# Kernel optimization log

Measured on AMD Instinct MI355X. Metric: run time of the kernel, lower is better.

## Reference

```python
import jax, jax.numpy as jnp
import numpy as np

N = 100000   # nodes
E = 1600000  # edges
IN = 128     # in_node_channels
H = 128      # hidden_channels
EPS = 1e-5   # BatchNorm eps


def _gcn_conv(x, W, b, src, dst, n):
    # x' = W x, then symmetric-normalized aggregation with self-loops (PyG GCNConv)
    xw = x @ W                                             # [N, H]
    loop = jnp.arange(n, dtype=src.dtype)
    src_f = jnp.concatenate([src, loop])                   # [E+N]
    dst_f = jnp.concatenate([dst, loop])
    deg = jax.ops.segment_sum(jnp.ones(src_f.shape, xw.dtype), dst_f, num_segments=n)
    dis = jax.lax.rsqrt(jnp.maximum(deg, 1.0))             # deg >= 1 due to self-loops
    norm = dis[src_f] * dis[dst_f]                         # [E+N]
    msg = xw[src_f] * norm[:, None]                        # gather + scale
    out = jax.ops.segment_sum(msg, dst_f, num_segments=n)  # scatter-add
    return out + b


def _bn(x, gamma, beta):
    # training-mode BatchNorm1d over the node dimension
    m = jnp.mean(x, axis=0)
    v = jnp.mean(jnp.square(x - m), axis=0)
    return gamma * (x - m) * jax.lax.rsqrt(v + EPS) + beta


def setup_inputs() -> dict:
    key = jax.random.key(0)
    ks = jax.random.split(key, 8)
    glorot = lambda k, shape, fan: jax.random.normal(k, shape, jnp.float32) / np.sqrt(fan).astype(np.float32)
    x = jax.random.normal(ks[0], (N, IN), jnp.float32)
    edge_index = jax.random.randint(ks[1], (2, E), 0, N, dtype=jnp.int32)
    return {
        "x": x,
        "edge_index": edge_index,
        "W1": glorot(ks[2], (IN, H), IN), "b1": jnp.zeros((H,), jnp.float32),
        "g1": jnp.ones((H,), jnp.float32), "be1": jnp.zeros((H,), jnp.float32),
        "W2": glorot(ks[3], (H, H), H), "b2": jnp.zeros((H,), jnp.float32),
        "g2": jnp.ones((H,), jnp.float32), "be2": jnp.zeros((H,), jnp.float32),
        "Wm1": glorot(ks[4], (H, 64), H), "bm1": jnp.zeros((64,), jnp.float32),
        "Wm2": glorot(ks[5], (64, 1), 64), "bm2": jnp.zeros((1,), jnp.float32),
    }


def reference(x, edge_index, W1, b1, g1, be1, W2, b2, g2, be2, Wm1, bm1, Wm2, bm2):
    src, dst = edge_index[0], edge_index[1]
    h = jax.nn.relu(_bn(_gcn_conv(x, W1, b1, src, dst, N), g1, be1))
    h = jax.nn.relu(_bn(_gcn_conv(h, W2, b2, src, dst, N), g2, be2))
    # MLP head (dropout is identity in eval / deterministic reference)
    h = jax.nn.relu(h @ Wm1 + bm1)
    out = h @ Wm2 + bm2                                     # [N, 1]
    return jnp.squeeze(out, axis=-1)                        # [N]
```

## Files before the change

kernel.cpp:

```cpp
#include <hip/hip_runtime.h>
#include <hip/hip_fp16.h>

#define HC 128
#define EPS_BN 1e-5f
#define NSTRIPE 8
#define AGG_BLOCKS 3072
#define BSHIFT 9
#define BNODES (1 << BSHIFT)
#define BCAP 12288
#define CHUNK 8192
#define SRC_BITS 18

typedef _Float16 f16;
typedef f16  f16x8 __attribute__((ext_vector_type(8)));
typedef float f32x4 __attribute__((ext_vector_type(4)));

__global__ __launch_bounds__(1024) void init_small(int* __restrict__ gcur,
                                                   float* __restrict__ stats,
                                                   f16* __restrict__ padrow) {
    int tid = threadIdx.x;
    if (tid < 256) gcur[tid] = tid * BCAP;
    if (tid < 128) padrow[tid] = (f16)0.f;
    for (int i = tid; i < 2 * NSTRIPE * 256; i += 1024) stats[i] = 0.f;
}

__global__ __launch_bounds__(1024) void edge_bin(const int* __restrict__ src,
                                                 const int* __restrict__ dst,
                                                 int* __restrict__ gcur,
                                                 unsigned int* __restrict__ packed, int E) {
    __shared__ int cnt[256];
    __shared__ int cur[256];
    const int tid = threadIdx.x;
    const int e0 = blockIdx.x * CHUNK;
    int dreg[8];
    if (tid < 256) cnt[tid] = 0;
    __syncthreads();
#pragma unroll
    for (int i = 0; i < 8; ++i) {
        int e = e0 + i * 1024 + tid;
        dreg[i] = (e < E) ? dst[e] : -1;
        if (dreg[i] >= 0) atomicAdd(&cnt[dreg[i] >> BSHIFT], 1);
    }
    __syncthreads();
    if (tid < 256) cur[tid] = (cnt[tid] > 0) ? atomicAdd(&gcur[tid], cnt[tid]) : 0;
    __syncthreads();
#pragma unroll
    for (int i = 0; i < 8; ++i) {
        int e = e0 + i * 1024 + tid;
        if (dreg[i] >= 0) {
            int s = src[e];
            int pos = atomicAdd(&cur[dreg[i] >> BSHIFT], 1);
            packed[pos] = ((unsigned)(dreg[i] & (BNODES - 1)) << SRC_BITS) | (unsigned)s;
        }
    }
}

__global__ __launch_bounds__(1024) void sort_wprep(const unsigned int* __restrict__ packed,
                                                   const int* __restrict__ gcur,
                                                   int2* __restrict__ rowptr2,
                                                   float* __restrict__ dis,
                                                   int* __restrict__ srcs, int n, int nbSort,
                                                   const float* __restrict__ W1,
                                                   const float* __restrict__ W2,
                                                   const float* __restrict__ Wm1,
                                                   f16* __restrict__ Wt1,
                                                   f16* __restrict__ Wt2,
                                                   f16* __restrict__ Wm1t) {
    if (blockIdx.x >= nbSort) {
        int idx = (blockIdx.x - nbSort) * 1024 + threadIdx.x;
        if (idx < 16384) {
            int k = idx >> 7, c = idx & 127;
            Wt1[(size_t)c * HC + k] = (f16)W1[idx];
        } else if (idx < 32768) {
            int i = idx - 16384;
            int k = i >> 7, c = i & 127;
            Wt2[(size_t)c * HC + k] = (f16)W2[i];
        } else if (idx < 40960) {
            int i = idx - 32768;
            int c = i >> 7, k = i & 127;
            Wm1t[(size_t)c * HC + k] = (f16)Wm1[(size_t)k * 64 + c];
        }
        return;
    }
    __shared__ int cnt[BNODES];
    __shared__ int cur[BNODES];
    __shared__ int scn[BNODES];
    const int b = blockIdx.x;
    const int node0 = b << BSHIFT;
    const int tid = threadIdx.x;
    const int base = b * BCAP;
    const int end  = gcur[b];

    if (tid < BNODES) cnt[tid] = 0;
    __syncthreads();
    for (int e = base + tid; e < end; e += 1024)
        atomicAdd(&cnt[packed[e] >> SRC_BITS], 1);
    __syncthreads();
    if (tid < BNODES) scn[tid] = cnt[tid];
    __syncthreads();
    for (int off = 1; off < BNODES; off <<= 1) {
        int t = 0;
        if (tid < BNODES && tid >= off) t = scn[tid - off];
        __syncthreads();
        if (tid < BNODES) scn[tid] += t;
        __syncthreads();
    }
    if (tid < BNODES) {
        int excl = scn[tid] - cnt[tid];
        int node = node0 + tid;
        if (node < n) {
            rowptr2[node] = make_int2(base + excl, base + excl + cnt[tid]);
            dis[node] = rsqrtf((float)cnt[tid] + 1.f);
        }
        cur[tid] = excl;
    }
    __syncthreads();
    for (int e = base + tid; e < end; e += 1024) {
        unsigned p = packed[e];
        int pos = atomicAdd(&cur[p >> SRC_BITS], 1);
        srcs[base + pos] = (int)(p & ((1u << SRC_BITS) - 1));
    }
}

template<int SRC_F16, int TRANS>
__global__ __launch_bounds__(512) void gemm_mfma(const void* __restrict__ Xv,
                                                 const f16* __restrict__ Wt,
                                                 const float* __restrict__ stats,
                                                 const float* __restrict__ gamma,
                                                 const float* __restrict__ beta,
                                                 const float* __restrict__ dis,
                                                 f16* __restrict__ Y, int n) {
    __shared__ f16 Ah[128][136];
    __shared__ f16 Bh[128][136];
    __shared__ float sc[HC], sh[HC];
    const int tid  = threadIdx.x;
    const int row0 = blockIdx.x * 128;

    if constexpr (TRANS) {
        if (tid < 128) {
            float s = 0.f, q = 0.f;
#pragma unroll
            for (int t = 0; t < NSTRIPE; ++t) {
                s += stats[t * 256 + tid];
                q += stats[t * 256 + 128 + tid];
            }
            float m = s / (float)n;
            float v = q / (float)n - m * m;
            float scv = gamma[tid] * rsqrtf(fmaxf(v, 0.f) + EPS_BN);
            sc[tid] = scv;
            sh[tid] = beta[tid] - m * scv;
        }
    }

#pragma unroll
    for (int i = 0; i < 4; ++i) {
        int idx = i * 512 + tid;
        int r = idx >> 4, g = idx & 15;
        *(f16x8*)&Bh[r][g * 8] = *(const f16x8*)(Wt + (size_t)r * HC + g * 8);
    }
    __syncthreads();

#pragma unroll
    for (int i = 0; i < 4; ++i) {
        int idx = i * 512 + tid;
        int r = idx >> 4, g = idx & 15;
        int grow = row0 + r;
        f16x8 h = {};
        if (grow < n) {
            if constexpr (SRC_F16) {
                f16x8 v = *(const f16x8*)((const f16*)Xv + (size_t)grow * HC + g * 8);
                if constexpr (TRANS) {
#pragma unroll
                    for (int j = 0; j < 8; ++j) {
                        float f = (float)v[j];
                        f = fmaxf(fmaf(f, sc[g * 8 + j], sh[g * 8 + j]), 0.f);
                        h[j] = (f16)f;
                    }
                } else h = v;
            } else {
                const float* X = (const float*)Xv;
                float4 a = *(const float4*)(X + (size_t)grow * HC + g * 8);
                float4 c = *(const float4*)(X + (size_t)grow * HC + g * 8 + 4);
                h[0] = (f16)a.x; h[1] = (f16)a.y; h[2] = (f16)a.z; h[3] = (f16)a.w;
                h[4] = (f16)c.x; h[5] = (f16)c.y; h[6] = (f16)c.z; h[7] = (f16)c.w;
            }
        }
        *(f16x8*)&Ah[r][g * 8] = h;
    }
    __syncthreads();

    const int wv   = tid >> 6;
    const int lane = tid & 63;
    const int m    = lane & 15;
    const int kq   = (lane >> 4) * 8;

    f32x4 acc[8] = {};
#pragma unroll
    for (int kc = 0; kc < HC; kc += 32) {
        f16x8 a = *(const f16x8*)&Ah[wv * 16 + m][kc + kq];
#pragma unroll
        for (int t = 0; t < 8; ++t) {
            f16x8 b = *(const f16x8*)&Bh[t * 16 + m][kc + kq];
            acc[t] = __builtin_amdgcn_mfma_f32_16x16x32_f16(a, b, acc[t], 0, 0, 0);
        }
    }

    __syncthreads();
    {
        const int rg = (lane >> 4) * 4;
        float dv[4];
#pragma unroll
        for (int r = 0; r < 4; ++r) {
            int grow = row0 + wv * 16 + rg + r;
            dv[r] = (grow < n) ? dis[grow] : 0.f;
        }
#pragma unroll
        for (int t = 0; t < 8; ++t)
#pragma unroll
            for (int r = 0; r < 4; ++r)
                Ah[wv * 16 + rg + r][t * 16 + m] = (f16)(acc[t][r] * dv[r]);
    }
    __syncthreads();
#pragma unroll
    for (int i = 0; i < 4; ++i) {
        int idx = i * 512 + tid;
        int r = idx >> 4, g = idx & 15;
        int grow = row0 + r;
        if (grow < n)
            *(f16x8*)(Y + (size_t)grow * HC + g * 8) = *(const f16x8*)&Ah[r][g * 8];
    }
}

__global__ __launch_bounds__(256) void gcn_agg_f16(const f16* __restrict__ xws,
                                                   const int* __restrict__ srcs,
                                                   const int2* __restrict__ rowptr2,
                                                   const float* __restrict__ dis,
                                                   const float* __restrict__ bias,
                                                   f16* __restrict__ out,
                                                   float* __restrict__ stats,
                                                   int n, int nwaves) {
    __shared__ float lds_s[4][128], lds_q[4][128];
    const int wv   = threadIdx.x >> 6;
    const int lane = threadIdx.x & 63;
    const int g    = lane >> 4;
    const int cg   = lane & 15;

    float b8[8];
#pragma unroll
    for (int j = 0; j < 8; ++j) b8[j] = bias[cg * 8 + j];

    float s8[8] = {}, q8[8] = {};

    for (int node = blockIdx.x * 4 + wv; node < n; node += nwaves) {
        const int2 rp = rowptr2[node];
        const int e1 = rp.y;
        float acc[8] = {};
        int e  = rp.x;
        int i0 = e + g, i1 = i0 + 4;
        int s0 = (i0 < e1) ? srcs[i0] : n;
        int s1 = (i1 < e1) ? srcs[i1] : n;
        while (e < e1) {
            int en = e + 8;
            int j0 = en + g, j1 = j0 + 4;
            int t0 = (j0 < e1) ? srcs[j0] : n;
            int t1 = (j1 < e1) ? srcs[j1] : n;
            f16x8 v0 = *(const f16x8*)(xws + (size_t)s0 * HC + cg * 8);
            f16x8 v1 = *(const f16x8*)(xws + (size_t)s1 * HC + cg * 8);
#pragma unroll
            for (int j = 0; j < 8; ++j) {
                acc[j] += (float)v0[j];
                acc[j] += (float)v1[j];
            }
            s0 = t0; s1 = t1; e = en;
        }
#pragma unroll
        for (int j = 0; j < 8; ++j) acc[j] += __shfl_xor(acc[j], 16);
#pragma unroll
        for (int j = 0; j < 8; ++j) acc[j] += __shfl_xor(acc[j], 32);

        if (g == 0) {
            float dv = dis[node];
            f16x8 self = *(const f16x8*)(xws + (size_t)node * HC + cg * 8);
            f16x8 o;
#pragma unroll
            for (int j = 0; j < 8; ++j) {
                float r = fmaf(acc[j] + (float)self[j], dv, b8[j]);
                o[j] = (f16)r;
                s8[j] += r;
                q8[j] += r * r;
            }
            *(f16x8*)(out + (size_t)node * HC + cg * 8) = o;
        }
    }

    if (g == 0) {
#pragma unroll
        for (int j = 0; j < 8; ++j) {
            lds_s[wv][cg * 8 + j] = s8[j];
            lds_q[wv][cg * 8 + j] = q8[j];
        }
    }
    __syncthreads();
    float* stripe = stats + (size_t)(blockIdx.x & (NSTRIPE - 1)) * 256;
    if (threadIdx.x < 128) {
        float s = lds_s[0][threadIdx.x] + lds_s[1][threadIdx.x] +
                  lds_s[2][threadIdx.x] + lds_s[3][threadIdx.x];
        float q = lds_q[0][threadIdx.x] + lds_q[1][threadIdx.x] +
                  lds_q[2][threadIdx.x] + lds_q[3][threadIdx.x];
        atomicAdd(&stripe[threadIdx.x], s);
        atomicAdd(&stripe[128 + threadIdx.x], q);
    }
}

__global__ __launch_bounds__(256) void mlp_mfma(const f16* __restrict__ h,
                                                const float* __restrict__ stats,
                                                const float* __restrict__ gamma,
                                                const float* __restrict__ beta,
                                                const f16* __restrict__ Wm1t,
                                                const float* __restrict__ bm1,
                                                const float* __restrict__ Wm2,
                                                const float* __restrict__ bm2,
                                                float* __restrict__ out, int n) {
    __shared__ f16 Hs[64][136];
    __shared__ f16 Ws[64][136];
    __shared__ float sc[HC], sh[HC], bmv[64], w2v[64];
    const int tid  = threadIdx.x;
    const int row0 = blockIdx.x * 64;

    if (tid < 128) {
        float s = 0.f, q = 0.f;
#pragma unroll
        for (int t = 0; t < NSTRIPE; ++t) {
            s += stats[t * 256 + tid];
            q += stats[t * 256 + 128 + tid];
        }
        float m = s / (float)n;
        float v = q / (float)n - m * m;
        float scv = gamma[tid] * rsqrtf(fmaxf(v, 0.f) + EPS_BN);
        sc[tid] = scv;
        sh[tid] = beta[tid] - m * scv;
    }
    if (tid < 64) { bmv[tid] = bm1[tid]; w2v[tid] = Wm2[tid]; }

#pragma unroll
    for (int i = 0; i < 4; ++i) {
        int idx = i * 256 + tid;
        int r = idx >> 4, g = idx & 15;
        *(f16x8*)&Ws[r][g * 8] = *(const f16x8*)(Wm1t + (size_t)r * HC + g * 8);
    }
    __syncthreads();

#pragma unroll
    for (int i = 0; i < 4; ++i) {
        int idx = i * 256 + tid;
        int r = idx >> 4, g = idx & 15;
        int grow = row0 + r;
        f16x8 hv = {};
        if (grow < n) {
            f16x8 v = *(const f16x8*)(h + (size_t)grow * HC + g * 8);
#pragma unroll
            for (int j = 0; j < 8; ++j) {
                float f = (float)v[j];
                f = fmaxf(fmaf(f, sc[g * 8 + j], sh[g * 8 + j]), 0.f);
                hv[j] = (f16)f;
            }
        }
        *(f16x8*)&Hs[r][g * 8] = hv;
    }
    __syncthreads();

    const int wv   = tid >> 6;
    const int lane = tid & 63;
    const int m    = lane & 15;
    const int kq   = (lane >> 4) * 8;

    f32x4 acc[4] = {};
#pragma unroll
    for (int kc = 0; kc < HC; kc += 32) {
        f16x8 a = *(const f16x8*)&Hs[wv * 16 + m][kc + kq];
#pragma unroll
        for (int t = 0; t < 4; ++t) {
            f16x8 b = *(const f16x8*)&Ws[t * 16 + m][kc + kq];
            acc[t] = __builtin_amdgcn_mfma_f32_16x16x32_f16(a, b, acc[t], 0, 0, 0);
        }
    }

    float part[4];
#pragma unroll
    for (int reg = 0; reg < 4; ++reg) {
        float s = 0.f;
#pragma unroll
        for (int t = 0; t < 4; ++t) {
            int col = t * 16 + m;
            s += fmaxf(acc[t][reg] + bmv[col], 0.f) * w2v[col];
        }
        part[reg] = s;
    }
#pragma unroll
    for (int off = 1; off < 16; off <<= 1) {
#pragma unroll
        for (int reg = 0; reg < 4; ++reg)
            part[reg] += __shfl_xor(part[reg], off);
    }
    if (m == 0) {
        int rbase = row0 + wv * 16 + (lane >> 4) * 4;
        float bb = bm2[0];
#pragma unroll
        for (int reg = 0; reg < 4; ++reg) {
            int row = rbase + reg;
            if (row < n) out[row] = part[reg] + bb;
        }
    }
}

extern "C" void kernel_launch(void* const* d_in, const int* in_sizes, int n_in,
                              void* d_out, int out_size, void* d_ws, size_t ws_size,
                              hipStream_t stream) {
    const float* x   = (const float*)d_in[0];
    const int*   ei  = (const int*)  d_in[1];
    const float* W1  = (const float*)d_in[2];
    const float* b1  = (const float*)d_in[3];
    const float* g1  = (const float*)d_in[4];
    const float* be1 = (const float*)d_in[5];
    const float* W2  = (const float*)d_in[6];
    const float* b2  = (const float*)d_in[7];
    const float* g2  = (const float*)d_in[8];
    const float* be2 = (const float*)d_in[9];
    const float* Wm1 = (const float*)d_in[10];
    const float* bm1 = (const float*)d_in[11];
    const float* Wm2 = (const float*)d_in[12];
    const float* bm2 = (const float*)d_in[13];
    float* out = (float*)d_out;

    const int n = in_sizes[0] / HC;
    const int E = in_sizes[1] / 2;
    const int* srcp = ei;
    const int* dstp = ei + E;
    const int nb = (n + BNODES - 1) >> BSHIFT;

    char* ws = (char*)d_ws;
    size_t off = 0;
    auto alloc = [&](size_t bytes) { void* p = ws + off; off = (off + bytes + 511) & ~511ULL; return p; };
    float*  dis     = (float*) alloc((size_t)n * 4);
    int2*   rowptr2 = (int2*)  alloc((size_t)n * 8);
    int*    gcur    = (int*)   alloc(1024);
    float*  stats   = (float*) alloc(2 * NSTRIPE * 256 * 4);
    float*  stats1  = stats;
    float*  stats2  = stats + NSTRIPE * 256;
    unsigned int* packed = (unsigned int*)alloc((size_t)nb * BCAP * 4);
    int*    srcs    = (int*)   alloc((size_t)nb * BCAP * 4);
    f16*    xws     = (f16*)   alloc((size_t)(n + 1) * HC * 2);
    f16*    bufBh   = (f16*)   alloc((size_t)n * HC * 2);
    f16*    Wt1     = (f16*)   alloc((size_t)HC * HC * 2);
    f16*    Wt2     = (f16*)   alloc((size_t)HC * HC * 2);
    f16*    Wm1t    = (f16*)   alloc((size_t)64 * HC * 2);

    const int gemmBlocks = (n + 127) / 128;
    const int mlpBlocks  = (n + 63) / 64;
    const int binBlocks  = (E + CHUNK - 1) / CHUNK;
    const int wprepBlks  = 40;
    const int aggWaves   = AGG_BLOCKS * 4;

    init_small<<<1, 1024, 0, stream>>>(gcur, stats, xws + (size_t)n * HC);

    edge_bin<<<binBlocks, 1024, 0, stream>>>(srcp, dstp, gcur, packed, E);
    sort_wprep<<<nb + wprepBlks, 1024, 0, stream>>>(packed, gcur, rowptr2, dis, srcs, n, nb,
                                                    W1, W2, Wm1, Wt1, Wt2, Wm1t);

    gemm_mfma<0, 0><<<gemmBlocks, 512, 0, stream>>>(x, Wt1, nullptr, nullptr, nullptr,
                                                    dis, xws, n);
    gcn_agg_f16<<<AGG_BLOCKS, 256, 0, stream>>>(xws, srcs, rowptr2, dis, b1,
                                                bufBh, stats1, n, aggWaves);

    gemm_mfma<1, 1><<<gemmBlocks, 512, 0, stream>>>(bufBh, Wt2, stats1, g1, be1,
                                                    dis, xws, n);
    gcn_agg_f16<<<AGG_BLOCKS, 256, 0, stream>>>(xws, srcs, rowptr2, dis, b2,
                                                bufBh, stats2, n, aggWaves);

    mlp_mfma<<<mlpBlocks, 256, 0, stream>>>(bufBh, stats2, g2, be2, Wm1t, bm1, Wm2, bm2,
                                            out, n);
}
```

Measured before the change: 310.7 us.

## Use finer edge buckets, smaller bin chunks, and 4-way unrolled aggregation gathers

Result: slower. 369.4 us (+18.9%).

```diff
diff --git a/kernel.cpp b/kernel.cpp
--- a/kernel.cpp
+++ b/kernel.cpp
@@ -4,11 +4,13 @@
 #define HC 128
 #define EPS_BN 1e-5f
 #define NSTRIPE 8
-#define AGG_BLOCKS 3072
-#define BSHIFT 9
+#define AGG_BLOCKS 2048
+#define BSHIFT 8
 #define BNODES (1 << BSHIFT)
-#define BCAP 12288
-#define CHUNK 8192
+#define NBMAX 512
+#define BCAP 6144
+#define CHUNK 4096
+#define EPT (CHUNK / 1024)
 #define SRC_BITS 18
 
 typedef _Float16 f16;
@@ -19,7 +21,7 @@
                                                    float* __restrict__ stats,
                                                    f16* __restrict__ padrow) {
     int tid = threadIdx.x;
-    if (tid < 256) gcur[tid] = tid * BCAP;
+    if (tid < NBMAX) gcur[tid] = tid * BCAP;
     if (tid < 128) padrow[tid] = (f16)0.f;
     for (int i = tid; i < 2 * NSTRIPE * 256; i += 1024) stats[i] = 0.f;
 }
@@ -28,24 +30,24 @@
                                                  const int* __restrict__ dst,
                                                  int* __restrict__ gcur,
                                                  unsigned int* __restrict__ packed, int E) {
-    __shared__ int cnt[256];
-    __shared__ int cur[256];
+    __shared__ int cnt[NBMAX];
+    __shared__ int cur[NBMAX];
     const int tid = threadIdx.x;
     const int e0 = blockIdx.x * CHUNK;
-    int dreg[8];
-    if (tid < 256) cnt[tid] = 0;
-    __syncthreads();
-#pragma unroll
-    for (int i = 0; i < 8; ++i) {
+    int dreg[EPT];
+    if (tid < NBMAX) cnt[tid] = 0;
+    __syncthreads();
+#pragma unroll
+    for (int i = 0; i < EPT; ++i) {
         int e = e0 + i * 1024 + tid;
         dreg[i] = (e < E) ? dst[e] : -1;
         if (dreg[i] >= 0) atomicAdd(&cnt[dreg[i] >> BSHIFT], 1);
     }
     __syncthreads();
-    if (tid < 256) cur[tid] = (cnt[tid] > 0) ? atomicAdd(&gcur[tid], cnt[tid]) : 0;
-    __syncthreads();
-#pragma unroll
-    for (int i = 0; i < 8; ++i) {
+    if (tid < NBMAX) cur[tid] = (cnt[tid] > 0) ? atomicAdd(&gcur[tid], cnt[tid]) : 0;
+    __syncthreads();
+#pragma unroll
+    for (int i = 0; i < EPT; ++i) {
         int e = e0 + i * 1024 + tid;
         if (dreg[i] >= 0) {
             int s = src[e];
@@ -231,19 +233,20 @@
     }
 }
 
-__global__ __launch_bounds__(256) void gcn_agg_f16(const f16* __restrict__ xws,
-                                                   const int* __restrict__ srcs,
-                                                   const int2* __restrict__ rowptr2,
-                                                   const float* __restrict__ dis,
-                                                   const float* __restrict__ bias,
-                                                   f16* __restrict__ out,
-                                                   float* __restrict__ stats,
-                                                   int n, int nwaves) {
+__global__ __launch_bounds__(256, 8) void gcn_agg_f16(const f16* __restrict__ xws,
+                                                      const int* __restrict__ srcs,
+                                                      const int2* __restrict__ rowptr2,
+                                                      const float* __restrict__ dis,
+                                                      const float* __restrict__ bias,
+                                                      f16* __restrict__ out,
+                                                      float* __restrict__ stats,
+                                                      int n, int nwaves) {
     __shared__ float lds_s[4][128], lds_q[4][128];
     const int wv   = threadIdx.x >> 6;
     const int lane = threadIdx.x & 63;
     const int g    = lane >> 4;
     const int cg   = lane & 15;
+    const unsigned coff = (unsigned)cg * 8;
 
     float b8[8];
 #pragma unroll
@@ -256,22 +259,26 @@
         const int e1 = rp.y;
         float acc[8] = {};
         int e  = rp.x;
-        int i0 = e + g, i1 = i0 + 4;
+        int i0 = e + g, i1 = i0 + 4, i2 = i0 + 8, i3 = i0 + 12;
         int s0 = (i0 < e1) ? srcs[i0] : n;
         int s1 = (i1 < e1) ? srcs[i1] : n;
+        int s2 = (i2 < e1) ? srcs[i2] : n;
+        int s3 = (i3 < e1) ? srcs[i3] : n;
         while (e < e1) {
-            int en = e + 8;
-            int j0 = en + g, j1 = j0 + 4;
+            int en = e + 16;
+            int j0 = en + g, j1 = j0 + 4, j2 = j0 + 8, j3 = j0 + 12;
             int t0 = (j0 < e1) ? srcs[j0] : n;
             int t1 = (j1 < e1) ? srcs[j1] : n;
-            f16x8 v0 = *(const f16x8*)(xws + (size_t)s0 * HC + cg * 8);
-            f16x8 v1 = *(const f16x8*)(xws + (size_t)s1 * HC + cg * 8);
-#pragma unroll
-            for (int j = 0; j < 8; ++j) {
-                acc[j] += (float)v0[j];
-                acc[j] += (float)v1[j];
-            }
-            s0 = t0; s1 = t1; e = en;
+            int t2 = (j2 < e1) ? srcs[j2] : n;
+            int t3 = (j3 < e1) ? srcs[j3] : n;
+            f16x8 v0 = *(const f16x8*)(xws + (unsigned)s0 * HC + coff);
+            f16x8 v1 = *(const f16x8*)(xws + (unsigned)s1 * HC + coff);
+            f16x8 v2 = *(const f16x8*)(xws + (unsigned)s2 * HC + coff);
+            f16x8 v3 = *(const f16x8*)(xws + (unsigned)s3 * HC + coff);
+#pragma unroll
+            for (int j = 0; j < 8; ++j)
+                acc[j] += ((float)v0[j] + (float)v1[j]) + ((float)v2[j] + (float)v3[j]);
+            s0 = t0; s1 = t1; s2 = t2; s3 = t3; e = en;
         }
 #pragma unroll
         for (int j = 0; j < 8; ++j) acc[j] += __shfl_xor(acc[j], 16);
@@ -280,7 +287,7 @@
 
         if (g == 0) {
             float dv = dis[node];
-            f16x8 self = *(const f16x8*)(xws + (size_t)node * HC + cg * 8);
+            f16x8 self = *(const f16x8*)(xws + (unsigned)node * HC + coff);
             f16x8 o;
 #pragma unroll
             for (int j = 0; j < 8; ++j) {
@@ -289,7 +296,7 @@
                 s8[j] += r;
                 q8[j] += r * r;
             }
-            *(f16x8*)(out + (size_t)node * HC + cg * 8) = o;
+            *(f16x8*)(out + (size_t)node * HC + coff) = o;
         }
     }
 
@@ -443,7 +450,7 @@
     auto alloc = [&](size_t bytes) { void* p = ws + off; off = (off + bytes + 511) & ~511ULL; return p; };
     float*  dis     = (float*) alloc((size_t)n * 4);
     int2*   rowptr2 = (int2*)  alloc((size_t)n * 8);
-    int*    gcur    = (int*)   alloc(1024);
+    int*    gcur    = (int*)   alloc(NBMAX * 4);
     float*  stats   = (float*) alloc(2 * NSTRIPE * 256 * 4);
     float*  stats1  = stats;
     float*  stats2  = stats + NSTRIPE * 256;
```

## Split node features into 16-channel planes and aggregate per channel chunk

Applied to the files above, without the earlier changes.

New measurement: 516.8 us. 66.4% more time.

```diff
diff --git a/kernel.cpp b/kernel.cpp
--- a/kernel.cpp
+++ b/kernel.cpp
@@ -2,9 +2,11 @@
 #include <hip/hip_fp16.h>
 
 #define HC 128
+#define CCH 16
+#define NCHUNK 8
 #define EPS_BN 1e-5f
 #define NSTRIPE 8
-#define AGG_BLOCKS 3072
+#define AGG_BLOCKS 2048
 #define BSHIFT 9
 #define BNODES (1 << BSHIFT)
 #define BCAP 12288
@@ -17,10 +19,13 @@
 
 __global__ __launch_bounds__(1024) void init_small(int* __restrict__ gcur,
                                                    float* __restrict__ stats,
-                                                   f16* __restrict__ padrow) {
+                                                   f16* __restrict__ xws, int n) {
     int tid = threadIdx.x;
     if (tid < 256) gcur[tid] = tid * BCAP;
-    if (tid < 128) padrow[tid] = (f16)0.f;
+    if (tid < NCHUNK * CCH) {
+        int ch = tid >> 4, c = tid & 15;
+        xws[(size_t)ch * ((size_t)(n + 1) * CCH) + (size_t)n * CCH + c] = (f16)0.f;
+    }
     for (int i = tid; i < 2 * NSTRIPE * 256; i += 1024) stats[i] = 0.f;
 }
 
@@ -135,6 +140,8 @@
     __shared__ float sc[HC], sh[HC];
     const int tid  = threadIdx.x;
     const int row0 = blockIdx.x * 128;
+    const size_t planeIn  = (size_t)n * CCH;
+    const size_t planeOut = (size_t)(n + 1) * CCH;
 
     if constexpr (TRANS) {
         if (tid < 128) {
@@ -168,7 +175,8 @@
         f16x8 h = {};
         if (grow < n) {
             if constexpr (SRC_F16) {
-                f16x8 v = *(const f16x8*)((const f16*)Xv + (size_t)grow * HC + g * 8);
+                f16x8 v = *(const f16x8*)((const f16*)Xv + (size_t)(g >> 1) * planeIn
+                                          + (size_t)grow * CCH + (g & 1) * 8);
                 if constexpr (TRANS) {
 #pragma unroll
                     for (int j = 0; j < 8; ++j) {
@@ -227,60 +235,62 @@
         int r = idx >> 4, g = idx & 15;
         int grow = row0 + r;
         if (grow < n)
-            *(f16x8*)(Y + (size_t)grow * HC + g * 8) = *(const f16x8*)&Ah[r][g * 8];
-    }
-}
-
-__global__ __launch_bounds__(256) void gcn_agg_f16(const f16* __restrict__ xws,
-                                                   const int* __restrict__ srcs,
-                                                   const int2* __restrict__ rowptr2,
-                                                   const float* __restrict__ dis,
-                                                   const float* __restrict__ bias,
-                                                   f16* __restrict__ out,
-                                                   float* __restrict__ stats,
-                                                   int n, int nwaves) {
-    __shared__ float lds_s[4][128], lds_q[4][128];
-    const int wv   = threadIdx.x >> 6;
-    const int lane = threadIdx.x & 63;
-    const int g    = lane >> 4;
-    const int cg   = lane & 15;
+            *(f16x8*)(Y + (size_t)(g >> 1) * planeOut + (size_t)grow * CCH + (g & 1) * 8)
+                = *(const f16x8*)&Ah[r][g * 8];
+    }
+}
+
+__global__ __launch_bounds__(256, 8) void gcn_agg_f16(const f16* __restrict__ xws,
+                                                      const int* __restrict__ srcs,
+                                                      const int2* __restrict__ rowptr2,
+                                                      const float* __restrict__ dis,
+                                                      const float* __restrict__ bias,
+                                                      f16* __restrict__ outC,
+                                                      float* __restrict__ stats,
+                                                      int n) {
+    __shared__ float lds_s[4][32], lds_q[4][32];
+    const int chunk = blockIdx.x & (NCHUNK - 1);
+    const int cblk  = blockIdx.x >> 3;
+    const int wv    = threadIdx.x >> 6;
+    const int lane  = threadIdx.x & 63;
+    const int sub   = lane >> 5;
+    const int g     = (lane >> 1) & 15;
+    const int cg    = lane & 1;
+    const f16* __restrict__ xp = xws + (size_t)chunk * ((size_t)(n + 1) * CCH);
+    f16* __restrict__ op = outC + (size_t)chunk * ((size_t)n * CCH);
 
     float b8[8];
 #pragma unroll
-    for (int j = 0; j < 8; ++j) b8[j] = bias[cg * 8 + j];
+    for (int j = 0; j < 8; ++j) b8[j] = bias[chunk * CCH + cg * 8 + j];
 
     float s8[8] = {}, q8[8] = {};
 
-    for (int node = blockIdx.x * 4 + wv; node < n; node += nwaves) {
-        const int2 rp = rowptr2[node];
-        const int e1 = rp.y;
+    for (int base = cblk * 8 + wv * 2; base < n; base += 2048) {
+        int node = base + sub;
+        bool valid = node < n;
+        int2 rp = rowptr2[valid ? node : (n - 1)];
+        if (!valid) rp.y = rp.x;
         float acc[8] = {};
-        int e  = rp.x;
-        int i0 = e + g, i1 = i0 + 4;
-        int s0 = (i0 < e1) ? srcs[i0] : n;
-        int s1 = (i1 < e1) ? srcs[i1] : n;
-        while (e < e1) {
-            int en = e + 8;
-            int j0 = en + g, j1 = j0 + 4;
-            int t0 = (j0 < e1) ? srcs[j0] : n;
-            int t1 = (j1 < e1) ? srcs[j1] : n;
-            f16x8 v0 = *(const f16x8*)(xws + (size_t)s0 * HC + cg * 8);
-            f16x8 v1 = *(const f16x8*)(xws + (size_t)s1 * HC + cg * 8);
-#pragma unroll
-            for (int j = 0; j < 8; ++j) {
-                acc[j] += (float)v0[j];
-                acc[j] += (float)v1[j];
-            }
-            s0 = t0; s1 = t1; e = en;
-        }
-#pragma unroll
-        for (int j = 0; j < 8; ++j) acc[j] += __shfl_xor(acc[j], 16);
-#pragma unroll
-        for (int j = 0; j < 8; ++j) acc[j] += __shfl_xor(acc[j], 32);
-
-        if (g == 0) {
+        int it = (rp.y - rp.x + 15) >> 4;
+        int itm = max(it, __shfl_xor(it, 32));
+        int e = rp.x + g;
+        int s0 = (e < rp.y) ? srcs[e] : n;
+        for (int k = 0; k < itm; ++k) {
+            int e2 = e + 16;
+            int s1 = (e2 < rp.y) ? srcs[e2] : n;
+            f16x8 v = *(const f16x8*)(xp + (size_t)s0 * CCH + cg * 8);
+#pragma unroll
+            for (int j = 0; j < 8; ++j) acc[j] += (float)v[j];
+            e = e2; s0 = s1;
+        }
+#pragma unroll
+        for (int off = 2; off <= 16; off <<= 1)
+#pragma unroll
+            for (int j = 0; j < 8; ++j) acc[j] += __shfl_xor(acc[j], off);
+
+        if (g == 0 && valid) {
             float dv = dis[node];
-            f16x8 self = *(const f16x8*)(xws + (size_t)node * HC + cg * 8);
+            f16x8 self = *(const f16x8*)(xp + (size_t)node * CCH + cg * 8);
             f16x8 o;
 #pragma unroll
             for (int j = 0; j < 8; ++j) {
@@ -289,26 +299,28 @@
                 s8[j] += r;
                 q8[j] += r * r;
             }
-            *(f16x8*)(out + (size_t)node * HC + cg * 8) = o;
+            *(f16x8*)(op + (size_t)node * CCH + cg * 8) = o;
         }
     }
 
     if (g == 0) {
 #pragma unroll
         for (int j = 0; j < 8; ++j) {
-            lds_s[wv][cg * 8 + j] = s8[j];
-            lds_q[wv][cg * 8 + j] = q8[j];
-        }
-    }
-    __syncthreads();
-    float* stripe = stats + (size_t)(blockIdx.x & (NSTRIPE - 1)) * 256;
-    if (threadIdx.x < 128) {
-        float s = lds_s[0][threadIdx.x] + lds_s[1][threadIdx.x] +
-                  lds_s[2][threadIdx.x] + lds_s[3][threadIdx.x];
-        float q = lds_q[0][threadIdx.x] + lds_q[1][threadIdx.x] +
-                  lds_q[2][threadIdx.x] + lds_q[3][threadIdx.x];
-        atomicAdd(&stripe[threadIdx.x], s);
-        atomicAdd(&stripe[128 + threadIdx.x], q);
+            lds_s[wv][sub * 16 + cg * 8 + j] = s8[j];
+            lds_q[wv][sub * 16 + cg * 8 + j] = q8[j];
+        }
+    }
+    __syncthreads();
+    float* stripe = stats + (size_t)((blockIdx.x >> 3) & (NSTRIPE - 1)) * 256;
+    if (threadIdx.x < 32) {
+        int ch = threadIdx.x & 15;
+        bool isq = threadIdx.x >= 16;
+        float v = 0.f;
+#pragma unroll
+        for (int w = 0; w < 4; ++w)
+            v += isq ? (lds_q[w][ch] + lds_q[w][16 + ch])
+                     : (lds_s[w][ch] + lds_s[w][16 + ch]);
+        atomicAdd(&stripe[(isq ? 128 : 0) + chunk * CCH + ch], v);
     }
 }
 
@@ -326,6 +338,7 @@
     __shared__ float sc[HC], sh[HC], bmv[64], w2v[64];
     const int tid  = threadIdx.x;
     const int row0 = blockIdx.x * 64;
+    const size_t planeIn = (size_t)n * CCH;
 
     if (tid < 128) {
         float s = 0.f, q = 0.f;
@@ -357,7 +370,8 @@
         int grow = row0 + r;
         f16x8 hv = {};
         if (grow < n) {
-            f16x8 v = *(const f16x8*)(h + (size_t)grow * HC + g * 8);
+            f16x8 v = *(const f16x8*)(h + (size_t)(g >> 1) * planeIn
+                                      + (size_t)grow * CCH + (g & 1) * 8);
 #pragma unroll
             for (int j = 0; j < 8; ++j) {
                 float f = (float)v[j];
@@ -449,8 +463,8 @@
     float*  stats2  = stats + NSTRIPE * 256;
     unsigned int* packed = (unsigned int*)alloc((size_t)nb * BCAP * 4);
     int*    srcs    = (int*)   alloc((size_t)nb * BCAP * 4);
-    f16*    xws     = (f16*)   alloc((size_t)(n + 1) * HC * 2);
-    f16*    bufBh   = (f16*)   alloc((size_t)n * HC * 2);
+    f16*    xws     = (f16*)   alloc((size_t)NCHUNK * (n + 1) * CCH * 2);
+    f16*    bufBh   = (f16*)   alloc((size_t)NCHUNK * n * CCH * 2);
     f16*    Wt1     = (f16*)   alloc((size_t)HC * HC * 2);
     f16*    Wt2     = (f16*)   alloc((size_t)HC * HC * 2);
     f16*    Wm1t    = (f16*)   alloc((size_t)64 * HC * 2);
@@ -459,9 +473,8 @@
     const int mlpBlocks  = (n + 63) / 64;
     const int binBlocks  = (E + CHUNK - 1) / CHUNK;
     const int wprepBlks  = 40;
-    const int aggWaves   = AGG_BLOCKS * 4;
-
-    init_small<<<1, 1024, 0, stream>>>(gcur, stats, xws + (size_t)n * HC);
+
+    init_small<<<1, 1024, 0, stream>>>(gcur, stats, xws, n);
 
     edge_bin<<<binBlocks, 1024, 0, stream>>>(srcp, dstp, gcur, packed, E);
     sort_wprep<<<nb + wprepBlks, 1024, 0, stream>>>(packed, gcur, rowptr2, dis, srcs, n, nb,
@@ -470,12 +483,12 @@
     gemm_mfma<0, 0><<<gemmBlocks, 512, 0, stream>>>(x, Wt1, nullptr, nullptr, nullptr,
                                                     dis, xws, n);
     gcn_agg_f16<<<AGG_BLOCKS, 256, 0, stream>>>(xws, srcs, rowptr2, dis, b1,
-                                                bufBh, stats1, n, aggWaves);
+                                                bufBh, stats1, n);
 
     gemm_mfma<1, 1><<<gemmBlocks, 512, 0, stream>>>(bufBh, Wt2, stats1, g1, be1,
                                                     dis, xws, n);
     gcn_agg_f16<<<AGG_BLOCKS, 256, 0, stream>>>(xws, srcs, rowptr2, dis, b2,
-                                                bufBh, stats2, n, aggWaves);
+                                                bufBh, stats2, n);
 
     mlp_mfma<<<mlpBlocks, 256, 0, stream>>>(bufBh, stats2, g2, be2, Wm1t, bm1, Wm2, bm2,
                                             out, n);
```
